# Kernel tuning notes

Measured on AMD Instinct MI355X. Metric: run time of the kernel, lower is better.

The kernel has to match this reference:

```python
import jax, jax.numpy as jnp
import numpy as np

N = 100000
E = 1200000
F_IN = 64
H = 64
C = 10


def _gcn_norm(edge_idx):
    # PyG gcn_norm with add_self_loops=True, edge_weight=1
    src = jnp.concatenate([edge_idx[0], jnp.arange(N, dtype=edge_idx.dtype)])
    dst = jnp.concatenate([edge_idx[1], jnp.arange(N, dtype=edge_idx.dtype)])
    deg = jax.ops.segment_sum(jnp.ones_like(dst, dtype=jnp.float32), dst, num_segments=N)
    dinv = jnp.where(deg > 0, jax.lax.rsqrt(deg), 0.0)
    norm = dinv[src] * dinv[dst]  # [E+N]
    return src, dst, norm


def _gcn_conv(x, src, dst, norm, W, b):
    h = x @ W                               # [N, out]
    msg = h[src] * norm[:, None]            # gather + scale, [E+N, out]
    out = jax.ops.segment_sum(msg, dst, num_segments=N)  # scatter-add
    return out + b


def setup_inputs() -> dict:
    key = jax.random.key(0)
    ks = jax.random.split(key, 8)
    x = jax.random.normal(ks[0], (N, F_IN), dtype=jnp.float32)
    edge_idx = jax.random.randint(ks[1], (2, E), 0, N, dtype=jnp.int64 if jax.config.jax_enable_x64 else jnp.int32)
    def glorot(k, fan_in, fan_out):
        s = jnp.sqrt(6.0 / (fan_in + fan_out)).astype(jnp.float32)
        return jax.random.uniform(k, (fan_in, fan_out), jnp.float32, -s, s)
    W0 = glorot(ks[2], F_IN, H); b0 = jnp.zeros((H,), jnp.float32)
    W1 = glorot(ks[3], H, H);    b1 = jnp.zeros((H,), jnp.float32)
    W2 = glorot(ks[4], H, H);    b2 = jnp.zeros((H,), jnp.float32)
    Wl = glorot(ks[5], H, C);    bl = jnp.zeros((C,), jnp.float32)
    return {"x": x, "edge_idx": edge_idx, "W0": W0, "b0": b0,
            "W1": W1, "b1": b1, "W2": W2, "b2": b2, "Wl": Wl, "bl": bl}


def reference(x, edge_idx, W0, b0, W1, b1, W2, b2, Wl, bl):
    src, dst, norm = _gcn_norm(edge_idx)
    # conv0 + relu
    h = jax.nn.relu(_gcn_conv(x, src, dst, norm, W0, b0))
    # convs[0] + relu (i=0 < num_layers-2=1)
    h = jax.nn.relu(_gcn_conv(h, src, dst, norm, W1, b1))
    # convs[1], no relu (last)
    h = _gcn_conv(h, src, dst, norm, W2, b2)
    # global_add_pool(batch=None): sum over all nodes, keepdim -> [1, H]
    g = jnp.sum(h, axis=0, keepdims=True)
    # dropout is identity in eval mode
    return g @ Wl + bl  # [1, C]
```

## Files before the change

### kernel.cpp

```cpp
#include <hip/hip_runtime.h>
#include <hip/hip_bf16.h>

#define NN 100000
#define NE 1200000
#define SCAN_B 256
#define NBLK ((NN + SCAN_B - 1) / SCAN_B)
#define NE4 (NE / 4)
#define XCD_N 8
#define NPX (NN / XCD_N)

__global__ __launch_bounds__(256) void count_kernel(const int* __restrict__ dst,
                                                    int* __restrict__ deg) {
    int xcd = blockIdx.x & 7;
    int sub = blockIdx.x >> 3;
    int nsub = gridDim.x >> 3;
    int lo = xcd * NPX;
    for (int i = sub * 256 + threadIdx.x; i < NE4; i += nsub * 256) {
        int4 d = ((const int4*)dst)[i];
        if ((unsigned)(d.x - lo) < NPX) atomicAdd(&deg[d.x], 1);
        if ((unsigned)(d.y - lo) < NPX) atomicAdd(&deg[d.y], 1);
        if ((unsigned)(d.z - lo) < NPX) atomicAdd(&deg[d.z], 1);
        if ((unsigned)(d.w - lo) < NPX) atomicAdd(&deg[d.w], 1);
    }
}

__global__ __launch_bounds__(SCAN_B) void scan1_kernel(const int* __restrict__ deg,
                                                       int* __restrict__ rowptr,
                                                       int* __restrict__ bsum,
                                                       float* __restrict__ dinv) {
    __shared__ int s[SCAN_B];
    int tid = threadIdx.x;
    int n = blockIdx.x * SCAN_B + tid;
    int d = (n < NN) ? deg[n] : 0;
    if (n < NN) dinv[n] = rsqrtf((float)(d + 1));
    s[tid] = d;
    for (int off = 1; off < SCAN_B; off <<= 1) {
        __syncthreads();
        int t = (tid >= off) ? s[tid - off] : 0;
        __syncthreads();
        s[tid] += t;
    }
    if (n <= NN) rowptr[n] = s[tid] - d;
    if (tid == SCAN_B - 1) bsum[blockIdx.x] = s[tid];
}

__global__ __launch_bounds__(512) void scan2_kernel(int* __restrict__ bsum,
                                                    int* __restrict__ boff) {
    __shared__ int s[512];
    int tid = threadIdx.x;
    int v = (tid < NBLK) ? bsum[tid] : 0;
    s[tid] = v;
    for (int off = 1; off < 512; off <<= 1) {
        __syncthreads();
        int t = (tid >= off) ? s[tid - off] : 0;
        __syncthreads();
        s[tid] += t;
    }
    if (tid < NBLK) boff[tid] = s[tid] - v;
}

__global__ __launch_bounds__(SCAN_B) void scan3_kernel(int* __restrict__ rowptr,
                                                       const int* __restrict__ boff,
                                                       int* __restrict__ rp2) {
    int n = blockIdx.x * SCAN_B + threadIdx.x;
    if (n < NN) {
        int v = rowptr[n] + boff[blockIdx.x];
        rowptr[n] = v;
        rp2[n] = v;
    }
    if (n == NN - 1) rowptr[NN] = NE;
}

__global__ __launch_bounds__(256) void fill_kernel(const int* __restrict__ src,
                                                   const int* __restrict__ dst,
                                                   int* __restrict__ rp2,
                                                   int* __restrict__ csr) {
    int xcd = blockIdx.x & 7;
    int sub = blockIdx.x >> 3;
    int nsub = gridDim.x >> 3;
    int lo = xcd * NPX;
    for (int i = sub * 256 + threadIdx.x; i < NE4; i += nsub * 256) {
        int4 d  = ((const int4*)dst)[i];
        int4 sr = ((const int4*)src)[i];
        if ((unsigned)(d.x - lo) < NPX) { int p = atomicAdd(&rp2[d.x], 1); csr[p] = sr.x; }
        if ((unsigned)(d.y - lo) < NPX) { int p = atomicAdd(&rp2[d.y], 1); csr[p] = sr.y; }
        if ((unsigned)(d.z - lo) < NPX) { int p = atomicAdd(&rp2[d.z], 1); csr[p] = sr.z; }
        if ((unsigned)(d.w - lo) < NPX) { int p = atomicAdd(&rp2[d.w], 1); csr[p] = sr.w; }
    }
}

template <int MODE>
__global__ __launch_bounds__(256) void mm_kernel(const float* __restrict__ in,
                                                 const float* __restrict__ W,
                                                 const float* __restrict__ bias,
                                                 const float* __restrict__ dinv,
                                                 __hip_bfloat16* __restrict__ u) {
    __shared__ float Ws[64 * 64];
    __shared__ float hrow[4][64];
    int tid = threadIdx.x;
    {
        const float4* Wv = (const float4*)W;
        float4* Wsv = (float4*)Ws;
        #pragma unroll
        for (int i = 0; i < 4; ++i) Wsv[tid + 256 * i] = Wv[tid + 256 * i];
    }
    int local = tid >> 6;
    int f = tid & 63;
    int n = blockIdx.x * 4 + local;
    float din = dinv[n];
    float v = in[n * 64 + f];
    if (MODE == 1) v = fmaxf(fmaf(din, v, bias[f]), 0.f);
    hrow[local][f] = v;
    __syncthreads();
    float acc = 0.f;
    #pragma unroll
    for (int k = 0; k < 64; ++k)
        acc = fmaf(hrow[local][k], Ws[k * 64 + f], acc);
    u[n * 64 + f] = __float2bfloat16(din * acc);
}

__device__ __forceinline__ void acc_bf8(float acc[8], uint4 v) {
    acc[0] += __uint_as_float(v.x << 16);
    acc[1] += __uint_as_float(v.x & 0xffff0000u);
    acc[2] += __uint_as_float(v.y << 16);
    acc[3] += __uint_as_float(v.y & 0xffff0000u);
    acc[4] += __uint_as_float(v.z << 16);
    acc[5] += __uint_as_float(v.z & 0xffff0000u);
    acc[6] += __uint_as_float(v.w << 16);
    acc[7] += __uint_as_float(v.w & 0xffff0000u);
}

__device__ __forceinline__ void agg_row(const int* __restrict__ rowptr,
                                        const int* __restrict__ csr,
                                        const uint4* __restrict__ u4,
                                        int n, int lane, int grp, int fo,
                                        float acc[8]) {
    float acc2[8];
    #pragma unroll
    for (int i = 0; i < 8; ++i) { acc[i] = 0.f; acc2[i] = 0.f; }
    int start = rowptr[n], end = rowptr[n + 1];
    int deg = end - start;
    int cidx = -1;
    if (lane < deg) cidx = csr[start + lane];
    if (grp == 0) acc_bf8(acc, u4[n * 8 + fo]);
    int s0 = __shfl(cidx, grp);
    int s1 = __shfl(cidx, grp + 8);
    if (grp < deg) acc_bf8(acc, u4[s0 * 8 + fo]);
    if (grp + 8 < deg) acc_bf8(acc2, u4[s1 * 8 + fo]);
    int dcap = deg < 64 ? deg : 64;
    for (int j = grp + 16; j < dcap; j += 8) {
        int s = __shfl(cidx, j);
        acc_bf8(acc, u4[s * 8 + fo]);
    }
    for (int base = start + 64; base < end; base += 64) {
        int bcnt = end - base; if (bcnt > 64) bcnt = 64;
        int c2 = (lane < bcnt) ? csr[base + lane] : -1;
        for (int j = grp; j < bcnt; j += 8) {
            int s = __shfl(c2, j);
            acc_bf8(acc2, u4[s * 8 + fo]);
        }
    }
    #pragma unroll
    for (int i = 0; i < 8; ++i) {
        float v = acc[i] + acc2[i];
        v += __shfl_xor(v, 8);
        v += __shfl_xor(v, 16);
        v += __shfl_xor(v, 32);
        acc[i] = v;
    }
}

template <int POOL>
__global__ __launch_bounds__(256) void agg_kernel(const int* __restrict__ rowptr,
                                                  const int* __restrict__ csr,
                                                  const uint4* __restrict__ uin,
                                                  const float* __restrict__ dinv,
                                                  float* __restrict__ a,
                                                  float* __restrict__ gp) {
    __shared__ float gpart[64];
    int tid = threadIdx.x;
    if (POOL) {
        if (tid < 64) gpart[tid] = 0.f;
        __syncthreads();
    }
    int lane = tid & 63;
    int grp = lane >> 3;
    int fo = lane & 7;
    int n = blockIdx.x * 4 + (tid >> 6);
    float acc[8];
    agg_row(rowptr, csr, uin, n, lane, grp, fo, acc);
    if (POOL) {
        if (grp == 0) {
            float din = dinv[n];
            #pragma unroll
            for (int i = 0; i < 8; ++i) atomicAdd(&gpart[fo * 8 + i], din * acc[i]);
        }
        __syncthreads();
        if (tid < 64) atomicAdd(&gp[(blockIdx.x & 63) * 64 + tid], gpart[tid]);
    } else {
        if (lane < 16) {
            float4 v = (lane < 8) ? make_float4(acc[0], acc[1], acc[2], acc[3])
                                  : make_float4(acc[4], acc[5], acc[6], acc[7]);
            ((float4*)a)[n * 16 + (lane & 7) * 2 + (lane >> 3)] = v;
        }
    }
}

__global__ __launch_bounds__(64) void head_kernel(const float* __restrict__ gp,
                                                  const float* __restrict__ b2,
                                                  const float* __restrict__ Wl,
                                                  const float* __restrict__ bl,
                                                  float* __restrict__ out) {
    int t = threadIdx.x;
    float s = 0.f;
    #pragma unroll 8
    for (int r = 0; r < 64; ++r) s += gp[r * 64 + t];
    float gf = s + (float)NN * b2[t];
    #pragma unroll
    for (int c = 0; c < 10; ++c) {
        float p = gf * Wl[t * 10 + c];
        #pragma unroll
        for (int off = 32; off > 0; off >>= 1) p += __shfl_down(p, off);
        if (t == 0) out[c] = p + bl[c];
    }
}

extern "C" void kernel_launch(void* const* d_in, const int* in_sizes, int n_in,
                              void* d_out, int out_size, void* d_ws, size_t ws_size,
                              hipStream_t stream) {
    const float* x  = (const float*)d_in[0];
    const int* eidx = (const int*)d_in[1];
    const int* esrc = eidx;
    const int* edst = eidx + NE;
    const float* W0 = (const float*)d_in[2];
    const float* b0 = (const float*)d_in[3];
    const float* W1 = (const float*)d_in[4];
    const float* b1 = (const float*)d_in[5];
    const float* W2 = (const float*)d_in[6];
    const float* b2 = (const float*)d_in[7];
    const float* Wl = (const float*)d_in[8];
    const float* bl = (const float*)d_in[9];
    float* out = (float*)d_out;

    float* ws = (float*)d_ws;
    size_t off = 0;
    int*   deg    = (int*)(ws + off); off += NN;
    float* dinv   =        ws + off;  off += NN;
    __hip_bfloat16* u = (__hip_bfloat16*)(ws + off); off += (size_t)NN * 32;
    float* a      =        ws + off;  off += (size_t)NN * 64;
    float* gp     =        ws + off;  off += 64 * 64;
    int*   rowptr = (int*)(ws + off); off += NN + 1;
    int*   rp2    = (int*)(ws + off); off += NN;
    int*   bsum   = (int*)(ws + off); off += 512;
    int*   boff   = (int*)(ws + off); off += 512;
    int*   csr    = (int*)(ws + off); off += NE;

    hipMemsetAsync(deg, 0, NN * sizeof(int), stream);
    hipMemsetAsync(gp, 0, 64 * 64 * sizeof(float), stream);

    count_kernel<<<2048, 256, 0, stream>>>(edst, deg);
    scan1_kernel<<<NBLK, SCAN_B, 0, stream>>>(deg, rowptr, bsum, dinv);
    scan2_kernel<<<1, 512, 0, stream>>>(bsum, boff);
    scan3_kernel<<<NBLK, SCAN_B, 0, stream>>>(rowptr, boff, rp2);
    fill_kernel<<<2048, 256, 0, stream>>>(esrc, edst, rp2, csr);

    mm_kernel<0><<<NN / 4, 256, 0, stream>>>(x, W0, nullptr, dinv, u);
    agg_kernel<0><<<NN / 4, 256, 0, stream>>>(rowptr, csr, (const uint4*)u, dinv, a, gp);
    mm_kernel<1><<<NN / 4, 256, 0, stream>>>(a, W1, b0, dinv, u);
    agg_kernel<0><<<NN / 4, 256, 0, stream>>>(rowptr, csr, (const uint4*)u, dinv, a, gp);
    mm_kernel<1><<<NN / 4, 256, 0, stream>>>(a, W2, b1, dinv, u);
    agg_kernel<1><<<NN / 4, 256, 0, stream>>>(rowptr, csr, (const uint4*)u, dinv, a, gp);
    head_kernel<<<1, 64, 0, stream>>>(gp, b2, Wl, bl, out);
}
```

Measured before the change: 400.5 us.

## Fuse CSR build into one cooperative kernel and store aggregates as bf16

Replaces the two memsets and five CSR-construction kernels (count, three scan stages, fill) with a single cooperative kernel that uses grid-wide syncs between phases. This removes launch overhead and inter-kernel gaps. The intermediate aggregation output is now stored as bf16 instead of fp32, halving its write and read traffic between the agg and mm kernels. The agg kernel also gets an occupancy hint in its launch bounds. The risks are the cost of grid syncs, lower CSR-build parallelism with 1024 blocks, and extra rounding error from bf16 intermediates.

```diff
diff --git a/kernel.cpp b/kernel.cpp
--- a/kernel.cpp
+++ b/kernel.cpp
@@ -1,5 +1,8 @@
 #include <hip/hip_runtime.h>
 #include <hip/hip_bf16.h>
+#include <hip/hip_cooperative_groups.h>
+
+namespace cg = cooperative_groups;
 
 #define NN 100000
 #define NE 1200000
@@ -8,80 +11,85 @@
 #define NE4 (NE / 4)
 #define XCD_N 8
 #define NPX (NN / XCD_N)
-
-__global__ __launch_bounds__(256) void count_kernel(const int* __restrict__ dst,
-                                                    int* __restrict__ deg) {
+#define BGRID 1024
+
+__global__ __launch_bounds__(256) void build_kernel(const int* __restrict__ esrc,
+                                                    const int* __restrict__ edst,
+                                                    int* __restrict__ deg,
+                                                    float* __restrict__ dinv,
+                                                    int* __restrict__ rowptr,
+                                                    int* __restrict__ rp2,
+                                                    int* __restrict__ bsum,
+                                                    int* __restrict__ boff,
+                                                    int* __restrict__ csr,
+                                                    float* __restrict__ gp) {
+    cg::grid_group grid = cg::this_grid();
+    __shared__ int s[512];
+    int tid = threadIdx.x;
+    int gidx = blockIdx.x * 256 + tid;
+    const int gstride = BGRID * 256;
     int xcd = blockIdx.x & 7;
     int sub = blockIdx.x >> 3;
-    int nsub = gridDim.x >> 3;
+    const int nsub = BGRID >> 3;
     int lo = xcd * NPX;
-    for (int i = sub * 256 + threadIdx.x; i < NE4; i += nsub * 256) {
-        int4 d = ((const int4*)dst)[i];
+
+    for (int i = gidx; i < NN; i += gstride) deg[i] = 0;
+    if (gidx < 64 * 64) gp[gidx] = 0.f;
+    grid.sync();
+
+    for (int i = sub * 256 + tid; i < NE4; i += nsub * 256) {
+        int4 d = ((const int4*)edst)[i];
         if ((unsigned)(d.x - lo) < NPX) atomicAdd(&deg[d.x], 1);
         if ((unsigned)(d.y - lo) < NPX) atomicAdd(&deg[d.y], 1);
         if ((unsigned)(d.z - lo) < NPX) atomicAdd(&deg[d.z], 1);
         if ((unsigned)(d.w - lo) < NPX) atomicAdd(&deg[d.w], 1);
     }
-}
-
-__global__ __launch_bounds__(SCAN_B) void scan1_kernel(const int* __restrict__ deg,
-                                                       int* __restrict__ rowptr,
-                                                       int* __restrict__ bsum,
-                                                       float* __restrict__ dinv) {
-    __shared__ int s[SCAN_B];
-    int tid = threadIdx.x;
-    int n = blockIdx.x * SCAN_B + tid;
-    int d = (n < NN) ? deg[n] : 0;
-    if (n < NN) dinv[n] = rsqrtf((float)(d + 1));
-    s[tid] = d;
-    for (int off = 1; off < SCAN_B; off <<= 1) {
+    grid.sync();
+
+    if (blockIdx.x < NBLK) {
+        int n = blockIdx.x * 256 + tid;
+        int d = (n < NN) ? deg[n] : 0;
+        if (n < NN) dinv[n] = rsqrtf((float)(d + 1));
+        s[tid] = d;
+        for (int off = 1; off < 256; off <<= 1) {
+            __syncthreads();
+            int t = (tid >= off) ? s[tid - off] : 0;
+            __syncthreads();
+            s[tid] += t;
+        }
+        if (n <= NN) rowptr[n] = s[tid] - d;
+        if (tid == 255) bsum[blockIdx.x] = s[tid];
+    }
+    grid.sync();
+
+    if (blockIdx.x == 0) {
+        int v0 = (tid < NBLK) ? bsum[tid] : 0;
+        int v1 = (tid + 256 < NBLK) ? bsum[tid + 256] : 0;
+        s[tid] = v0; s[tid + 256] = v1;
         __syncthreads();
-        int t = (tid >= off) ? s[tid - off] : 0;
-        __syncthreads();
-        s[tid] += t;
-    }
-    if (n <= NN) rowptr[n] = s[tid] - d;
-    if (tid == SCAN_B - 1) bsum[blockIdx.x] = s[tid];
-}
-
-__global__ __launch_bounds__(512) void scan2_kernel(int* __restrict__ bsum,
-                                                    int* __restrict__ boff) {
-    __shared__ int s[512];
-    int tid = threadIdx.x;
-    int v = (tid < NBLK) ? bsum[tid] : 0;
-    s[tid] = v;
-    for (int off = 1; off < 512; off <<= 1) {
-        __syncthreads();
-        int t = (tid >= off) ? s[tid - off] : 0;
-        __syncthreads();
-        s[tid] += t;
-    }
-    if (tid < NBLK) boff[tid] = s[tid] - v;
-}
-
-__global__ __launch_bounds__(SCAN_B) void scan3_kernel(int* __restrict__ rowptr,
-                                                       const int* __restrict__ boff,
-                                                       int* __restrict__ rp2) {
-    int n = blockIdx.x * SCAN_B + threadIdx.x;
-    if (n < NN) {
-        int v = rowptr[n] + boff[blockIdx.x];
+        for (int off = 1; off < 512; off <<= 1) {
+            int a0 = (tid >= off) ? s[tid - off] : 0;
+            int a1 = (tid + 256 >= off) ? s[tid + 256 - off] : 0;
+            __syncthreads();
+            s[tid] += a0; s[tid + 256] += a1;
+            __syncthreads();
+        }
+        if (tid < NBLK) boff[tid] = s[tid] - v0;
+        if (tid + 256 < NBLK) boff[tid + 256] = s[tid + 256] - v1;
+    }
+    grid.sync();
+
+    for (int n = gidx; n < NN; n += gstride) {
+        int v = rowptr[n] + boff[n >> 8];
         rowptr[n] = v;
         rp2[n] = v;
     }
-    if (n == NN - 1) rowptr[NN] = NE;
-}
-
-__global__ __launch_bounds__(256) void fill_kernel(const int* __restrict__ src,
-                                                   const int* __restrict__ dst,
-                                                   int* __restrict__ rp2,
-                                                   int* __restrict__ csr) {
-    int xcd = blockIdx.x & 7;
-    int sub = blockIdx.x >> 3;
-    int nsub = gridDim.x >> 3;
-    int lo = xcd * NPX;
-    for (int i = sub * 256 + threadIdx.x; i < NE4; i += nsub * 256) {
-        int4 d  = ((const int4*)dst)[i];
-        int4 sr = ((const int4*)src)[i];
+    if (gidx == 0) rowptr[NN] = NE;
+    grid.sync();
+
+    for (int i = sub * 256 + tid; i < NE4; i += nsub * 256) {
+        int4 d  = ((const int4*)edst)[i];
+        int4 sr = ((const int4*)esrc)[i];
         if ((unsigned)(d.x - lo) < NPX) { int p = atomicAdd(&rp2[d.x], 1); csr[p] = sr.x; }
         if ((unsigned)(d.y - lo) < NPX) { int p = atomicAdd(&rp2[d.y], 1); csr[p] = sr.y; }
         if ((unsigned)(d.z - lo) < NPX) { int p = atomicAdd(&rp2[d.z], 1); csr[p] = sr.z; }
@@ -90,7 +98,7 @@
 }
 
 template <int MODE>
-__global__ __launch_bounds__(256) void mm_kernel(const float* __restrict__ in,
+__global__ __launch_bounds__(256) void mm_kernel(const void* __restrict__ in,
                                                  const float* __restrict__ W,
                                                  const float* __restrict__ bias,
                                                  const float* __restrict__ dinv,
@@ -108,8 +116,13 @@
     int f = tid & 63;
     int n = blockIdx.x * 4 + local;
     float din = dinv[n];
-    float v = in[n * 64 + f];
-    if (MODE == 1) v = fmaxf(fmaf(din, v, bias[f]), 0.f);
+    float v;
+    if (MODE == 0) {
+        v = ((const float*)in)[n * 64 + f];
+    } else {
+        v = __bfloat162float(((const __hip_bfloat16*)in)[n * 64 + f]);
+        v = fmaxf(fmaf(din, v, bias[f]), 0.f);
+    }
     hrow[local][f] = v;
     __syncthreads();
     float acc = 0.f;
@@ -128,6 +141,14 @@
     acc[5] += __uint_as_float(v.z & 0xffff0000u);
     acc[6] += __uint_as_float(v.w << 16);
     acc[7] += __uint_as_float(v.w & 0xffff0000u);
+}
+
+__device__ __forceinline__ unsigned packbf2(float lof, float hif) {
+    __hip_bfloat16 l = __float2bfloat16(lof), h = __float2bfloat16(hif);
+    unsigned short ul, uh;
+    __builtin_memcpy(&ul, &l, 2);
+    __builtin_memcpy(&uh, &h, 2);
+    return ((unsigned)uh << 16) | ul;
 }
 
 __device__ __forceinline__ void agg_row(const int* __restrict__ rowptr,
@@ -171,12 +192,12 @@
 }
 
 template <int POOL>
-__global__ __launch_bounds__(256) void agg_kernel(const int* __restrict__ rowptr,
-                                                  const int* __restrict__ csr,
-                                                  const uint4* __restrict__ uin,
-                                                  const float* __restrict__ dinv,
-                                                  float* __restrict__ a,
-                                                  float* __restrict__ gp) {
+__global__ __launch_bounds__(256, 8) void agg_kernel(const int* __restrict__ rowptr,
+                                                     const int* __restrict__ csr,
+                                                     const uint4* __restrict__ uin,
+                                                     const float* __restrict__ dinv,
+                                                     __hip_bfloat16* __restrict__ a,
+                                                     float* __restrict__ gp) {
     __shared__ float gpart[64];
     int tid = threadIdx.x;
     if (POOL) {
@@ -198,10 +219,13 @@
         __syncthreads();
         if (tid < 64) atomicAdd(&gp[(blockIdx.x & 63) * 64 + tid], gpart[tid]);
     } else {
-        if (lane < 16) {
-            float4 v = (lane < 8) ? make_float4(acc[0], acc[1], acc[2], acc[3])
-                                  : make_float4(acc[4], acc[5], acc[6], acc[7]);
-            ((float4*)a)[n * 16 + (lane & 7) * 2 + (lane >> 3)] = v;
+        if (grp == 0) {
+            uint4 pv;
+            pv.x = packbf2(acc[0], acc[1]);
+            pv.y = packbf2(acc[2], acc[3]);
+            pv.z = packbf2(acc[4], acc[5]);
+            pv.w = packbf2(acc[6], acc[7]);
+            ((uint4*)a)[n * 8 + fo] = pv;
         }
     }
 }
@@ -230,8 +254,8 @@
                               hipStream_t stream) {
     const float* x  = (const float*)d_in[0];
     const int* eidx = (const int*)d_in[1];
-    const int* esrc = eidx;
-    const int* edst = eidx + NE;
+    const int* esrc = (const int*)eidx;
+    const int* edst = (const int*)eidx + NE;
     const float* W0 = (const float*)d_in[2];
     const float* b0 = (const float*)d_in[3];
     const float* W1 = (const float*)d_in[4];
@@ -247,7 +271,7 @@
     int*   deg    = (int*)(ws + off); off += NN;
     float* dinv   =        ws + off;  off += NN;
     __hip_bfloat16* u = (__hip_bfloat16*)(ws + off); off += (size_t)NN * 32;
-    float* a      =        ws + off;  off += (size_t)NN * 64;
+    __hip_bfloat16* a = (__hip_bfloat16*)(ws + off); off += (size_t)NN * 32;
     float* gp     =        ws + off;  off += 64 * 64;
     int*   rowptr = (int*)(ws + off); off += NN + 1;
     int*   rp2    = (int*)(ws + off); off += NN;
@@ -255,14 +279,13 @@
     int*   boff   = (int*)(ws + off); off += 512;
     int*   csr    = (int*)(ws + off); off += NE;
 
-    hipMemsetAsync(deg, 0, NN * sizeof(int), stream);
-    hipMemsetAsync(gp, 0, 64 * 64 * sizeof(float), stream);
-
-    count_kernel<<<2048, 256, 0, stream>>>(edst, deg);
-    scan1_kernel<<<NBLK, SCAN_B, 0, stream>>>(deg, rowptr, bsum, dinv);
-    scan2_kernel<<<1, 512, 0, stream>>>(bsum, boff);
-    scan3_kernel<<<NBLK, SCAN_B, 0, stream>>>(rowptr, boff, rp2);
-    fill_kernel<<<2048, 256, 0, stream>>>(esrc, edst, rp2, csr);
+    {
+        void* args[] = {(void*)&esrc, (void*)&edst, (void*)&deg, (void*)&dinv,
+                        (void*)&rowptr, (void*)&rp2, (void*)&bsum, (void*)&boff,
+                        (void*)&csr, (void*)&gp};
+        hipLaunchCooperativeKernel((void*)build_kernel, dim3(BGRID), dim3(256),
+                                   args, 0, stream);
+    }
 
     mm_kernel<0><<<NN / 4, 256, 0, stream>>>(x, W0, nullptr, dinv, u);
     agg_kernel<0><<<NN / 4, 256, 0, stream>>>(rowptr, csr, (const uint4*)u, dinv, a, gp);
```

Result: slower. 863.4 us (+115.6%).
